# Kernel optimization log

Hardware: AMD Instinct MI355X
Metric: run time of the kernel (lower is better)

Reference implementation:

```python
import jax, jax.numpy as jnp
import numpy as np

B, S, D = 4, 2048, 2048
H, DH = 16, 128


def setup_inputs() -> dict:
    key = jax.random.key(0)
    k1, k2, k3, k4, k5 = jax.random.split(key, 5)
    x = jax.random.normal(k1, (B, S, D), dtype=jnp.float32)
    # causal mask, broadcast over heads and batch (module does mask.unsqueeze(0))
    attn_mask = jnp.tril(jnp.ones((S, S), dtype=jnp.int32))
    # torch Linear weights: [out, in]; scaled like default init
    w_qkv = jax.random.normal(k2, (3 * H * DH, D), dtype=jnp.float32) / np.sqrt(D)
    b_qkv = jax.random.normal(k3, (3 * H * DH,), dtype=jnp.float32) * 0.01
    w_out = jax.random.normal(k4, (D, H * DH), dtype=jnp.float32) / np.sqrt(H * DH)
    b_out = jax.random.normal(k5, (D,), dtype=jnp.float32) * 0.01
    return {"x": x, "attn_mask": attn_mask, "w_qkv": w_qkv, "b_qkv": b_qkv,
            "w_out": w_out, "b_out": b_out}


def reference(x, attn_mask, w_qkv, b_qkv, w_out, b_out):
    b, s, d = x.shape
    qkv = x @ w_qkv.T + b_qkv                      # [B,S,3*H*DH]
    qkv = qkv.reshape(b, s, H, 3 * DH)             # per-head contiguous 3*DH slice
    qkv = jnp.transpose(qkv, (2, 0, 1, 3))         # [H,B,S,3*DH]
    q, k, v = jnp.split(qkv, 3, axis=-1)           # each [H,B,S,DH]
    scores = jnp.einsum('hbqd,hbkd->hbqk', q, k) / np.sqrt(DH)
    scores = jnp.where(attn_mask[None, None] == 0, -jnp.inf, scores)
    attn = jax.nn.softmax(scores, axis=-1)         # dropout is identity at eval
    ctx = jnp.einsum('hbqk,hbkd->hbqd', attn, v)   # [H,B,S,DH]
    ctx = jnp.transpose(ctx, (1, 2, 0, 3)).reshape(b, s, H * DH)
    return ctx @ w_out.T + b_out
```

## Files before the change

### kernel.cpp

```cpp
#include <hip/hip_runtime.h>

typedef unsigned short u16;
typedef __bf16 bf16x8 __attribute__((ext_vector_type(8)));
typedef unsigned short u16x8 __attribute__((ext_vector_type(8)));
typedef float f32x4 __attribute__((ext_vector_type(4)));

#define GLDS16(gp, lp)                                                        \
  __builtin_amdgcn_global_load_lds(                                           \
      (const __attribute__((address_space(1))) void*)(gp),                    \
      (__attribute__((address_space(3))) void*)(lp), 16, 0, 0)

__device__ __forceinline__ u16 f2bf(float f) {
  unsigned u = __float_as_uint(f);
  u += 0x7FFFu + ((u >> 16) & 1u);
  return (u16)(u >> 16);
}

__device__ __forceinline__ f32x4 mfma_bf16(bf16x8 a, bf16x8 b, f32x4 c) {
  return __builtin_amdgcn_mfma_f32_16x16x32_bf16(a, b, c, 0, 0, 0);
}

__global__ void cvt_f32_bf16(const float* __restrict__ src,
                             u16* __restrict__ dst, int n8) {
  for (int i = blockIdx.x * blockDim.x + threadIdx.x; i < n8;
       i += gridDim.x * blockDim.x) {
    const float4* sp = (const float4*)src + (size_t)i * 2;
    float4 a = sp[0], b = sp[1];
    u16x8 o;
    o[0] = f2bf(a.x); o[1] = f2bf(a.y); o[2] = f2bf(a.z); o[3] = f2bf(a.w);
    o[4] = f2bf(b.x); o[5] = f2bf(b.y); o[6] = f2bf(b.z); o[7] = f2bf(b.w);
    *((u16x8*)dst + i) = o;
  }
}

template <int OUT_BF16>
__global__ __launch_bounds__(256) void gemm_bt(const u16* __restrict__ A,
                                               const u16* __restrict__ B,
                                               const float* __restrict__ bias,
                                               void* __restrict__ Cout, int M,
                                               int N, int K) {
  __shared__ __attribute__((aligned(16))) u16 As[128 * 64];
  __shared__ __attribute__((aligned(16))) u16 Bs[128 * 64];
  const int t = threadIdx.x, lane = t & 63, w = t >> 6;
  const int l15 = lane & 15, l4 = lane >> 4;
  const int bm = blockIdx.x * 128, bn = blockIdx.y * 128;
  const int wr = (w >> 1) * 64, wc = (w & 1) * 64;

  f32x4 z4 = {0.f, 0.f, 0.f, 0.f};
  f32x4 acc[4][4];
#pragma unroll
  for (int i = 0; i < 4; ++i)
#pragma unroll
    for (int j = 0; j < 4; ++j) acc[i][j] = z4;

  const int srow = t >> 3;
  const int scol = ((t & 7) ^ (srow & 7)) << 3;
  const u16* Ag = A + (size_t)(bm + srow) * K + scol;
  const u16* Bg = B + (size_t)(bn + srow) * K + scol;
  u16* AsW = As + w * 512;
  u16* BsW = Bs + w * 512;

  for (int k0 = 0; k0 < K; k0 += 64) {
    __syncthreads();
#pragma unroll
    for (int i = 0; i < 4; ++i) {
      GLDS16(Ag + k0 + i * 32 * K, AsW + i * 2048);
      GLDS16(Bg + k0 + i * 32 * K, BsW + i * 2048);
    }
    __syncthreads();
#pragma unroll
    for (int kc = 0; kc < 2; ++kc) {
      bf16x8 af[4], bf[4];
#pragma unroll
      for (int x = 0; x < 4; ++x) {
        int ra = wr + x * 16 + l15;
        af[x] = *(const bf16x8*)(As + ra * 64 + (((kc * 4 + l4) ^ (ra & 7)) << 3));
        int rb = wc + x * 16 + l15;
        bf[x] = *(const bf16x8*)(Bs + rb * 64 + (((kc * 4 + l4) ^ (rb & 7)) << 3));
      }
#pragma unroll
      for (int mi = 0; mi < 4; ++mi)
#pragma unroll
        for (int ni = 0; ni < 4; ++ni)
          acc[mi][ni] = mfma_bf16(af[mi], bf[ni], acc[mi][ni]);
    }
  }
  const int cr = l4 * 4, cc = l15;
#pragma unroll
  for (int ni = 0; ni < 4; ++ni) {
    int col = bn + wc + ni * 16 + cc;
    float bv = bias[col];
#pragma unroll
    for (int mi = 0; mi < 4; ++mi)
#pragma unroll
      for (int r = 0; r < 4; ++r) {
        int row = bm + wr + mi * 16 + cr + r;
        float v = acc[mi][ni][r] + bv;
        if (OUT_BF16)
          ((u16*)Cout)[(size_t)row * N + col] = f2bf(v);
        else
          ((float*)Cout)[(size_t)row * N + col] = v;
      }
  }
}

__global__ __launch_bounds__(256) void attn_fwd(const u16* __restrict__ qkv,
                                                u16* __restrict__ ctx) {
  constexpr int NQ = 6144, SD = 2048;
  __shared__ __attribute__((aligned(16))) u16 Ks[64 * 128];
  __shared__ __attribute__((aligned(16))) u16 Vt[128 * 72];
  __shared__ __attribute__((aligned(16))) u16 Ps[64 * 72];
  const int t = threadIdx.x, lane = t & 63, w = t >> 6;
  const int l15 = lane & 15, l4 = lane >> 4;
  const int q0 = blockIdx.x * 64;
  const int h = blockIdx.y, b = blockIdx.z;
  const size_t rowbase = (size_t)b * SD;
  const int hq = h * 384;

  bf16x8 qf[4];
  {
    const u16* qp = qkv + (rowbase + q0 + w * 16 + l15) * NQ + hq + l4 * 8;
#pragma unroll
    for (int kc = 0; kc < 4; ++kc) qf[kc] = *(const bf16x8*)(qp + kc * 32);
  }

  f32x4 z4 = {0.f, 0.f, 0.f, 0.f};
  f32x4 oacc[8];
#pragma unroll
  for (int i = 0; i < 8; ++i) oacc[i] = z4;
  float m_run[4], l_run[4];
#pragma unroll
  for (int r = 0; r < 4; ++r) { m_run[r] = -3.0e38f; l_run[r] = 0.f; }

  const u16* Kg = qkv + (rowbase + (t >> 4)) * NQ + hq + 128 +
                  (((t & 15) ^ ((t >> 4) & 7)) << 3);
  const u16* Vg = qkv + (rowbase + (t & 15)) * NQ + hq + 256 + ((t >> 4) << 3);
  const int vkk = t & 15, vd0 = (t >> 4) << 3;

  const float scale = 0.08838834764831845f;
  const int qrow = q0 + w * 16 + l4 * 4;

  for (int k0 = 0; k0 <= q0; k0 += 64) {
    __syncthreads();
#pragma unroll
    for (int i = 0; i < 4; ++i)
      GLDS16(Kg + (size_t)(k0 + i * 16) * NQ, Ks + i * 2048 + w * 512);
#pragma unroll
    for (int p = 0; p < 4; ++p) {
      u16x8 v = *(const u16x8*)(Vg + (size_t)(k0 + p * 16) * NQ);
      int kk = p * 16 + vkk;
#pragma unroll
      for (int j = 0; j < 8; ++j) Vt[(vd0 + j) * 72 + kk] = v[j];
    }
    __syncthreads();

    f32x4 sc[4];
#pragma unroll
    for (int nf = 0; nf < 4; ++nf) sc[nf] = z4;
#pragma unroll
    for (int kc = 0; kc < 4; ++kc)
#pragma unroll
      for (int nf = 0; nf < 4; ++nf) {
        int rk = nf * 16 + l15;
        bf16x8 kf =
            *(const bf16x8*)(Ks + rk * 128 + (((kc * 4 + l4) ^ (rk & 7)) << 3));
        sc[nf] = mfma_bf16(qf[kc], kf, sc[nf]);
      }
#pragma unroll
    for (int nf = 0; nf < 4; ++nf) {
      int col = k0 + nf * 16 + l15;
#pragma unroll
      for (int r = 0; r < 4; ++r) {
        float s = sc[nf][r] * scale;
        sc[nf][r] = (col > qrow + r) ? -3.0e38f : s;
      }
    }
    float mx[4], sm[4];
#pragma unroll
    for (int r = 0; r < 4; ++r)
      mx[r] = fmaxf(fmaxf(sc[0][r], sc[1][r]), fmaxf(sc[2][r], sc[3][r]));
#pragma unroll
    for (int off = 8; off >= 1; off >>= 1)
#pragma unroll
      for (int r = 0; r < 4; ++r) mx[r] = fmaxf(mx[r], __shfl_xor(mx[r], off));
    float corr[4];
#pragma unroll
    for (int r = 0; r < 4; ++r) {
      float mn = fmaxf(m_run[r], mx[r]);
      corr[r] = __expf(m_run[r] - mn);
      m_run[r] = mn;
    }
#pragma unroll
    for (int nf = 0; nf < 4; ++nf)
#pragma unroll
      for (int r = 0; r < 4; ++r) sc[nf][r] = __expf(sc[nf][r] - m_run[r]);
#pragma unroll
    for (int r = 0; r < 4; ++r)
      sm[r] = (sc[0][r] + sc[1][r]) + (sc[2][r] + sc[3][r]);
#pragma unroll
    for (int off = 8; off >= 1; off >>= 1)
#pragma unroll
      for (int r = 0; r < 4; ++r) sm[r] += __shfl_xor(sm[r], off);
#pragma unroll
    for (int r = 0; r < 4; ++r) l_run[r] = l_run[r] * corr[r] + sm[r];
#pragma unroll
    for (int nf = 0; nf < 8; ++nf)
#pragma unroll
      for (int r = 0; r < 4; ++r) oacc[nf][r] *= corr[r];
#pragma unroll
    for (int nf = 0; nf < 4; ++nf)
#pragma unroll
      for (int r = 0; r < 4; ++r)
        Ps[(w * 16 + l4 * 4 + r) * 72 + nf * 16 + l15] = f2bf(sc[nf][r]);
    __syncthreads();
#pragma unroll
    for (int kc = 0; kc < 2; ++kc) {
      bf16x8 pf = *(const bf16x8*)(Ps + (w * 16 + l15) * 72 + kc * 32 + l4 * 8);
#pragma unroll
      for (int nf = 0; nf < 8; ++nf) {
        bf16x8 vf =
            *(const bf16x8*)(Vt + (nf * 16 + l15) * 72 + kc * 32 + l4 * 8);
        oacc[nf] = mfma_bf16(pf, vf, oacc[nf]);
      }
    }
  }
  float inv[4];
#pragma unroll
  for (int r = 0; r < 4; ++r) inv[r] = 1.f / l_run[r];
  u16* cp = ctx + (rowbase + q0 + w * 16 + l4 * 4) * SD + h * 128 + l15;
#pragma unroll
  for (int nf = 0; nf < 8; ++nf)
#pragma unroll
    for (int r = 0; r < 4; ++r)
      cp[(size_t)r * SD + nf * 16] = f2bf(oacc[nf][r] * inv[r]);
}

extern "C" void kernel_launch(void* const* d_in, const int* in_sizes, int n_in,
                              void* d_out, int out_size, void* d_ws,
                              size_t ws_size, hipStream_t stream) {
  const float* x = (const float*)d_in[0];
  const float* wqkv = (const float*)d_in[2];
  const float* bqkv = (const float*)d_in[3];
  const float* wout = (const float*)d_in[4];
  const float* bout = (const float*)d_in[5];
  float* out = (float*)d_out;
  char* ws = (char*)d_ws;

  u16* xb = (u16*)(ws);
  u16* wqkvb = (u16*)(ws + 33554432);
  u16* woutb = (u16*)(ws + 58720256);
  u16* qkvb = (u16*)(ws + 67108864);
  u16* ctx = xb;

  cvt_f32_bf16<<<2048, 256, 0, stream>>>(x, xb, 16777216 / 8);
  cvt_f32_bf16<<<2048, 256, 0, stream>>>(wqkv, wqkvb, 12582912 / 8);
  cvt_f32_bf16<<<1024, 256, 0, stream>>>(wout, woutb, 4194304 / 8);
  gemm_bt<1><<<dim3(64, 48), 256, 0, stream>>>(xb, wqkvb, bqkv, qkvb, 8192,
                                               6144, 2048);
  attn_fwd<<<dim3(32, 16, 4), 256, 0, stream>>>(qkvb, ctx);
  gemm_bt<0><<<dim3(64, 16), 256, 0, stream>>>(ctx, woutb, bout, out, 8192,
                                               2048, 2048);
}
```

Baseline: 739.4 us.

## Tune causal attention: lazy rescale, exp2 softmax, XOR-swizzled LDS, reversed block order

The attention kernel now applies the causal mask only on the diagonal tile and folds the softmax scale into an exp2 constant. It rescales the running max and accumulators only when some row's max grows past a threshold, in the lazy-rescaling style. Vt and Ps drop their padded layouts for XOR-swizzled ones and use native bf16 conversion. Q blocks are launched in reverse so the longest causal rows go first, and the barrier between writing and reading Ps is removed because each wave reads only its own rows. The goal is less VALU work, fewer barriers and better load balance, at the cost of a bounded overflow margin in the lazy rescale.

```diff
diff --git a/kernel.cpp b/kernel.cpp
--- a/kernel.cpp
+++ b/kernel.cpp
@@ -104,15 +104,22 @@
   }
 }
 
+__device__ __forceinline__ int vt_idx(int d, int kk) {
+  return d * 64 + ((((kk >> 3) ^ ((d >> 3) & 7)) << 3) | (kk & 7));
+}
+__device__ __forceinline__ int ps_idx(int r, int c) {
+  return r * 64 + ((((c >> 3) ^ ((r >> 2) & 7)) << 3) | (c & 7));
+}
+
 __global__ __launch_bounds__(256) void attn_fwd(const u16* __restrict__ qkv,
                                                 u16* __restrict__ ctx) {
   constexpr int NQ = 6144, SD = 2048;
   __shared__ __attribute__((aligned(16))) u16 Ks[64 * 128];
-  __shared__ __attribute__((aligned(16))) u16 Vt[128 * 72];
-  __shared__ __attribute__((aligned(16))) u16 Ps[64 * 72];
+  __shared__ __attribute__((aligned(16))) u16 Vt[128 * 64];
+  __shared__ __attribute__((aligned(16))) u16 Ps[64 * 64];
   const int t = threadIdx.x, lane = t & 63, w = t >> 6;
   const int l15 = lane & 15, l4 = lane >> 4;
-  const int q0 = blockIdx.x * 64;
+  const int q0 = (int)(gridDim.x - 1 - blockIdx.x) * 64;
   const int h = blockIdx.y, b = blockIdx.z;
   const size_t rowbase = (size_t)b * SD;
   const int hq = h * 384;
@@ -137,7 +144,8 @@
   const u16* Vg = qkv + (rowbase + (t & 15)) * NQ + hq + 256 + ((t >> 4) << 3);
   const int vkk = t & 15, vd0 = (t >> 4) << 3;
 
-  const float scale = 0.08838834764831845f;
+  const float C = 0.12751879522447905f;
+  const float THRC = 8.0f / 0.12751879522447905f;
   const int qrow = q0 + w * 16 + l4 * 4;
 
   for (int k0 = 0; k0 <= q0; k0 += 64) {
@@ -150,7 +158,7 @@
       u16x8 v = *(const u16x8*)(Vg + (size_t)(k0 + p * 16) * NQ);
       int kk = p * 16 + vkk;
 #pragma unroll
-      for (int j = 0; j < 8; ++j) Vt[(vd0 + j) * 72 + kk] = v[j];
+      for (int j = 0; j < 8; ++j) Vt[vt_idx(vd0 + j, kk)] = v[j];
     }
     __syncthreads();
 
@@ -166,16 +174,16 @@
             *(const bf16x8*)(Ks + rk * 128 + (((kc * 4 + l4) ^ (rk & 7)) << 3));
         sc[nf] = mfma_bf16(qf[kc], kf, sc[nf]);
       }
-#pragma unroll
-    for (int nf = 0; nf < 4; ++nf) {
-      int col = k0 + nf * 16 + l15;
-#pragma unroll
-      for (int r = 0; r < 4; ++r) {
-        float s = sc[nf][r] * scale;
-        sc[nf][r] = (col > qrow + r) ? -3.0e38f : s;
-      }
-    }
-    float mx[4], sm[4];
+    if (k0 == q0) {
+#pragma unroll
+      for (int nf = 0; nf < 4; ++nf) {
+        int col = k0 + nf * 16 + l15;
+#pragma unroll
+        for (int r = 0; r < 4; ++r)
+          if (col > qrow + r) sc[nf][r] = -3.0e38f;
+      }
+    }
+    float mx[4];
 #pragma unroll
     for (int r = 0; r < 4; ++r)
       mx[r] = fmaxf(fmaxf(sc[0][r], sc[1][r]), fmaxf(sc[2][r], sc[3][r]));
@@ -183,17 +191,28 @@
     for (int off = 8; off >= 1; off >>= 1)
 #pragma unroll
       for (int r = 0; r < 4; ++r) mx[r] = fmaxf(mx[r], __shfl_xor(mx[r], off));
-    float corr[4];
-#pragma unroll
-    for (int r = 0; r < 4; ++r) {
-      float mn = fmaxf(m_run[r], mx[r]);
-      corr[r] = __expf(m_run[r] - mn);
-      m_run[r] = mn;
-    }
+    bool upd = false;
+#pragma unroll
+    for (int r = 0; r < 4; ++r) upd |= (mx[r] > m_run[r] + THRC);
+    if (__any(upd)) {
+#pragma unroll
+      for (int r = 0; r < 4; ++r) {
+        float mn = fmaxf(m_run[r], mx[r]);
+        float cr = exp2f((m_run[r] - mn) * C);
+        m_run[r] = mn;
+        l_run[r] *= cr;
+#pragma unroll
+        for (int nf = 0; nf < 8; ++nf) oacc[nf][r] *= cr;
+      }
+    }
+    float mC[4], sm[4];
+#pragma unroll
+    for (int r = 0; r < 4; ++r) mC[r] = m_run[r] * C;
 #pragma unroll
     for (int nf = 0; nf < 4; ++nf)
 #pragma unroll
-      for (int r = 0; r < 4; ++r) sc[nf][r] = __expf(sc[nf][r] - m_run[r]);
+      for (int r = 0; r < 4; ++r)
+        sc[nf][r] = exp2f(fmaf(sc[nf][r], C, -mC[r]));
 #pragma unroll
     for (int r = 0; r < 4; ++r)
       sm[r] = (sc[0][r] + sc[1][r]) + (sc[2][r] + sc[3][r]);
@@ -202,24 +221,21 @@
 #pragma unroll
       for (int r = 0; r < 4; ++r) sm[r] += __shfl_xor(sm[r], off);
 #pragma unroll
-    for (int r = 0; r < 4; ++r) l_run[r] = l_run[r] * corr[r] + sm[r];
-#pragma unroll
-    for (int nf = 0; nf < 8; ++nf)
-#pragma unroll
-      for (int r = 0; r < 4; ++r) oacc[nf][r] *= corr[r];
+    for (int r = 0; r < 4; ++r) l_run[r] += sm[r];
 #pragma unroll
     for (int nf = 0; nf < 4; ++nf)
 #pragma unroll
       for (int r = 0; r < 4; ++r)
-        Ps[(w * 16 + l4 * 4 + r) * 72 + nf * 16 + l15] = f2bf(sc[nf][r]);
-    __syncthreads();
+        ((__bf16*)Ps)[ps_idx(w * 16 + l4 * 4 + r, nf * 16 + l15)] =
+            (__bf16)sc[nf][r];
 #pragma unroll
     for (int kc = 0; kc < 2; ++kc) {
-      bf16x8 pf = *(const bf16x8*)(Ps + (w * 16 + l15) * 72 + kc * 32 + l4 * 8);
+      bf16x8 pf = *(const bf16x8*)(
+          Ps + ps_idx(w * 16 + l15, kc * 32 + l4 * 8));
 #pragma unroll
       for (int nf = 0; nf < 8; ++nf) {
         bf16x8 vf =
-            *(const bf16x8*)(Vt + (nf * 16 + l15) * 72 + kc * 32 + l4 * 8);
+            *(const bf16x8*)(Vt + vt_idx(nf * 16 + l15, kc * 32 + l4 * 8));
         oacc[nf] = mfma_bf16(pf, vf, oacc[nf]);
       }
     }
@@ -232,7 +248,7 @@
   for (int nf = 0; nf < 8; ++nf)
 #pragma unroll
     for (int r = 0; r < 4; ++r)
-      cp[(size_t)r * SD + nf * 16] = f2bf(oacc[nf][r] * inv[r]);
+      ((__bf16*)cp)[(size_t)r * SD + nf * 16] = (__bf16)(oacc[nf][r] * inv[r]);
 }
 
 extern "C" void kernel_launch(void* const* d_in, const int* in_sizes, int n_in,
```

Measured after the change: 787.3 us. +6.5%, slower.
